# Performance work log

Measured on AMD Instinct MI355X. Metric: run time of the kernel, lower is better.

## Reference

```python
import jax, jax.numpy as jnp
import numpy as np

N = 100000      # num nodes
E = 500000      # num edges
IN_DIM = 128
OUT_DIM = 128
H = 8           # n_heads
DK = OUT_DIM // H  # 16


def setup_inputs() -> dict:
    key = jax.random.key(0)
    ks = jax.random.split(key, 16)
    s = 1.0 / np.sqrt(IN_DIM)
    inp = {
        "x": jax.random.normal(ks[0], (N, IN_DIM), dtype=jnp.float32),
        "edge_index": jax.random.randint(ks[1], (2, E), 0, N, dtype=jnp.int64),
        # per-type linear layers (num_types=1)
        "Wk": jax.random.uniform(ks[2], (OUT_DIM, IN_DIM), jnp.float32, -s, s),
        "bk": jnp.zeros((OUT_DIM,), jnp.float32),
        "Wq": jax.random.uniform(ks[3], (OUT_DIM, IN_DIM), jnp.float32, -s, s),
        "bq": jnp.zeros((OUT_DIM,), jnp.float32),
        "Wv": jax.random.uniform(ks[4], (OUT_DIM, IN_DIM), jnp.float32, -s, s),
        "bv": jnp.zeros((OUT_DIM,), jnp.float32),
        "Wa": jax.random.uniform(ks[5], (OUT_DIM, OUT_DIM), jnp.float32, -s, s),
        "ba": jnp.zeros((OUT_DIM,), jnp.float32),
        # per-relation params (num_relations=1), xavier-uniform for d_k x d_k mats
        "R_att": jax.random.uniform(ks[6], (H, DK, DK), jnp.float32, -np.sqrt(6.0 / (2 * DK)), np.sqrt(6.0 / (2 * DK))),
        "R_msg": jax.random.uniform(ks[7], (H, DK, DK), jnp.float32, -np.sqrt(6.0 / (2 * DK)), np.sqrt(6.0 / (2 * DK))),
        "R_pri": jnp.ones((H,), jnp.float32),
        "skip": jnp.ones((), jnp.float32),
    }
    return inp


def reference(x, edge_index, Wk, bk, Wq, bq, Wv, bv, Wa, ba, R_att, R_msg, R_pri, skip):
    sqrt_dk = jnp.asarray(np.sqrt(DK), x.dtype)
    # per-node projections -> [N, H, DK]
    k = (x @ Wk.T + bk).reshape(N, H, DK)
    q = (x @ Wq.T + bq).reshape(N, H, DK)
    v = (x @ Wv.T + bv).reshape(N, H, DK)
    src, dst = edge_index[0], edge_index[1]
    # edge gather: [E, H, DK]
    ke = jnp.einsum('ehd,hdf->ehf', k[src], R_att)
    ve = jnp.einsum('ehd,hdf->ehf', v[src], R_msg)
    qe = q[dst]
    # attention scores [E, H]; softmax over the edge axis (as in the original)
    att = jnp.sum(qe * ke, axis=-1) * R_pri / sqrt_dk
    att = jax.nn.softmax(att, axis=0)
    # weighted sum over all edges -> [H, DK] -> [OUT_DIM]
    out = jnp.einsum('eh,ehf->hf', att, ve).reshape(-1)
    out = Wa @ out + ba  # a_linear on the pooled vector
    alpha = jax.nn.sigmoid(skip)
    # broadcast skip mix against node inputs -> [N, OUT_DIM]
    return out * alpha + x * (1.0 - alpha)
```

## Files before the change

kernel.cpp:

```cpp
#include <hip/hip_runtime.h>
#include <hip/hip_bf16.h>

#define NN 100000
#define EE 500000
#define NB2 256
#define EGRID 2048

typedef __attribute__((ext_vector_type(8))) __bf16 bf16x8;
typedef __attribute__((ext_vector_type(4))) float f32x4;
typedef __attribute__((ext_vector_type(2))) float f32x2;

static const long long OFF_KQ8  = 0;
static const long long OFF_VB   = 6400000;
static const long long OFF_WGT  = 12800000;
static const long long OFF_PART = 13600000;
static const long long OFF_OUTV = 13634816;
static const long long OFF_CNT  = 13634944;

__device__ inline unsigned short f2bf(float f) {
    unsigned int u = __float_as_uint(f);
    unsigned int r = (u + 0x7FFFu + ((u >> 16) & 1u)) >> 16;
    return (unsigned short)r;
}
__device__ inline unsigned int pack2bf(float a, float b) {
    return (unsigned int)f2bf(a) | ((unsigned int)f2bf(b) << 16);
}
#define LOF(u) __uint_as_float((u) << 16)
#define HIF(u) __uint_as_float((u) & 0xffff0000u)

#if __has_builtin(__builtin_amdgcn_cvt_pk_fp8_f32) && __has_builtin(__builtin_amdgcn_cvt_pk_f32_fp8)
#define HW_FP8 1
#endif

__device__ inline unsigned char enc_fp8(float f) {
#ifdef HW_FP8
    int p = __builtin_amdgcn_cvt_pk_fp8_f32(f, f, 0, false);
    return (unsigned char)(p & 0xff);
#else
    unsigned int u = __float_as_uint(f);
    unsigned int s = (u >> 24) & 0x80u;
    unsigned int a = u & 0x7fffffffu;
    if (a >= 0x43e80000u) return (unsigned char)(s | 0x7e);
    if (a < 0x3c800000u) {
        float av = __uint_as_float(a);
        unsigned int m = (unsigned int)rintf(av * 512.0f);
        return (unsigned char)(s | m);
    }
    unsigned int base = a - 0x3c000000u;
    unsigned int r = (base + 0x7ffffu + ((base >> 20) & 1u)) >> 20;
    return (unsigned char)(s | r);
#endif
}

#ifndef HW_FP8
__device__ inline float dec1_fp8(unsigned int b) {
    unsigned int s = (b & 0x80u) << 24;
    unsigned int em = b & 0x7fu;
    float v;
    if (em >= 8u) v = __uint_as_float(s | ((em + 960u) << 20));
    else {
        v = (float)em * 0.001953125f;
        v = __uint_as_float(__float_as_uint(v) | s);
    }
    return v;
}
#endif

__device__ inline float dot4_fp8(unsigned int ka, unsigned int qa, float d) {
#ifdef HW_FP8
    f32x2 k0 = __builtin_amdgcn_cvt_pk_f32_fp8((int)ka, false);
    f32x2 k1 = __builtin_amdgcn_cvt_pk_f32_fp8((int)ka, true);
    f32x2 q0 = __builtin_amdgcn_cvt_pk_f32_fp8((int)qa, false);
    f32x2 q1 = __builtin_amdgcn_cvt_pk_f32_fp8((int)qa, true);
    d = fmaf(k0.x, q0.x, d); d = fmaf(k0.y, q0.y, d);
    d = fmaf(k1.x, q1.x, d); d = fmaf(k1.y, q1.y, d);
    return d;
#else
    #pragma unroll
    for (int i = 0; i < 4; ++i)
        d = fmaf(dec1_fp8((ka >> (8*i)) & 0xff), dec1_fp8((qa >> (8*i)) & 0xff), d);
    return d;
#endif
}

__global__ __launch_bounds__(512) void proj_all(const float* __restrict__ x,
                                                const float* __restrict__ Wk, const float* __restrict__ bk,
                                                const float* __restrict__ Wq, const float* __restrict__ bq,
                                                const float* __restrict__ Wv, const float* __restrict__ bv,
                                                const float* __restrict__ R_att,
                                                unsigned char* __restrict__ kq8,
                                                unsigned char* __restrict__ vb,
                                                float* __restrict__ Wgt,
                                                unsigned int* __restrict__ counter) {
    __shared__ __align__(16) char smem[131072];
    unsigned short* As = (unsigned short*)smem;
    unsigned short* Bs = (unsigned short*)(smem + 32768);
    int tid = threadIdx.x;
    long long row0 = (long long)blockIdx.x * 128;

    {
        long long zidx = (long long)blockIdx.x * 512 + tid;
        if (zidx < 200000) ((float4*)Wgt)[zidx] = make_float4(0.f, 0.f, 0.f, 0.f);
        if (blockIdx.x == 0 && tid == 0) *counter = 0u;
    }

    for (int c = tid; c < 2048; c += 512) {
        int r = c >> 4, sl = c & 15;
        long long gr = row0 + r;
        float4 v0, v1;
        if (gr < NN) {
            const float4* xp = (const float4*)(x + gr * 128 + sl * 8);
            v0 = xp[0]; v1 = xp[1];
        } else {
            v0 = make_float4(0.f, 0.f, 0.f, 0.f);
            v1 = make_float4(0.f, 0.f, 0.f, 0.f);
        }
        uint4 pk;
        pk.x = pack2bf(v0.x, v0.y); pk.y = pack2bf(v0.z, v0.w);
        pk.z = pack2bf(v1.x, v1.y); pk.w = pack2bf(v1.z, v1.w);
        *(uint4*)(As + r * 128 + (sl ^ (r & 15)) * 8) = pk;
    }
    for (int c = tid; c < 6144; c += 512) {
        int r = c >> 4, sl = c & 15;
        int cc = sl * 8;
        float w0,w1,w2,w3,w4,w5,w6,w7;
        if (r < 128) {
            float4 a = *(const float4*)(Wk + r * 128 + cc);
            float4 b = *(const float4*)(Wk + r * 128 + cc + 4);
            w0=a.x; w1=a.y; w2=a.z; w3=a.w; w4=b.x; w5=b.y; w6=b.z; w7=b.w;
        } else if (r < 256) {
            int h = (r - 128) >> 4, d = (r - 128) & 15;
            const float* Rrow = R_att + h * 256 + d * 16;
            w0=w1=w2=w3=w4=w5=w6=w7 = 0.f;
            #pragma unroll
            for (int f = 0; f < 16; ++f) {
                float rv = Rrow[f];
                const float* wq = Wq + (h * 16 + f) * 128 + cc;
                float4 a = *(const float4*)wq;
                float4 b = *(const float4*)(wq + 4);
                w0 = fmaf(rv, a.x, w0); w1 = fmaf(rv, a.y, w1);
                w2 = fmaf(rv, a.z, w2); w3 = fmaf(rv, a.w, w3);
                w4 = fmaf(rv, b.x, w4); w5 = fmaf(rv, b.y, w5);
                w6 = fmaf(rv, b.z, w6); w7 = fmaf(rv, b.w, w7);
            }
        } else {
            float4 a = *(const float4*)(Wv + (r - 256) * 128 + cc);
            float4 b = *(const float4*)(Wv + (r - 256) * 128 + cc + 4);
            w0=a.x; w1=a.y; w2=a.z; w3=a.w; w4=b.x; w5=b.y; w6=b.z; w7=b.w;
        }
        uint4 pk;
        pk.x = pack2bf(w0, w1); pk.y = pack2bf(w2, w3);
        pk.z = pack2bf(w4, w5); pk.w = pack2bf(w6, w7);
        *(uint4*)(Bs + r * 128 + (sl ^ (r & 15)) * 8) = pk;
    }
    __syncthreads();

    int lane = tid & 63, wv = tid >> 6, wr = wv >> 2, wc = wv & 3;
    int lrow = lane & 15, lk = lane >> 4;
    f32x4 acc[4][6];
    #pragma unroll
    for (int m = 0; m < 4; ++m)
        #pragma unroll
        for (int n = 0; n < 6; ++n)
            acc[m][n] = f32x4{0.f, 0.f, 0.f, 0.f};

    #pragma unroll
    for (int kk = 0; kk < 4; ++kk) {
        int kc = kk * 4 + lk;
        bf16x8 a[4], b[6];
        #pragma unroll
        for (int m = 0; m < 4; ++m) {
            int r = wr * 64 + m * 16 + lrow;
            a[m] = *(const bf16x8*)(As + r * 128 + (kc ^ (r & 15)) * 8);
        }
        #pragma unroll
        for (int n = 0; n < 6; ++n) {
            int r = wc * 96 + n * 16 + lrow;
            b[n] = *(const bf16x8*)(Bs + r * 128 + (kc ^ (r & 15)) * 8);
        }
        #pragma unroll
        for (int m = 0; m < 4; ++m)
            #pragma unroll
            for (int n = 0; n < 6; ++n)
                acc[m][n] = __builtin_amdgcn_mfma_f32_16x16x32_bf16(a[m], b[n], acc[m][n], 0, 0, 0);
    }
    __syncthreads();

    unsigned char* CsK = (unsigned char*)smem;
    unsigned short* CsV = (unsigned short*)(smem + 32768);
    float bias[6];
    #pragma unroll
    for (int n = 0; n < 6; ++n) {
        int cb = wc * 96 + n * 16 + lrow;
        if (cb < 128) bias[n] = bk[cb];
        else if (cb < 256) {
            int h = (cb - 128) >> 4, d = (cb - 128) & 15;
            float s = 0.f;
            #pragma unroll
            for (int f = 0; f < 16; ++f)
                s = fmaf(R_att[h * 256 + d * 16 + f], bq[h * 16 + f], s);
            bias[n] = s;
        } else bias[n] = bv[cb - 256];
    }
    #pragma unroll
    for (int m = 0; m < 4; ++m) {
        int rb = wr * 64 + m * 16 + lk * 4;
        #pragma unroll
        for (int n = 0; n < 6; ++n) {
            int cb = wc * 96 + n * 16 + lrow;
            if (cb < 256) {
                #pragma unroll
                for (int r = 0; r < 4; ++r)
                    CsK[(rb + r) * 256 + cb] = enc_fp8(acc[m][n][r] + bias[n]);
            } else {
                #pragma unroll
                for (int r = 0; r < 4; ++r)
                    CsV[(rb + r) * 128 + (cb - 256)] = f2bf(acc[m][n][r] + bias[n]);
            }
        }
    }
    __syncthreads();
    for (int c = tid; c < 2048; c += 512) {
        int r = c >> 4, sl = c & 15;
        long long gr = row0 + r;
        if (gr < NN)
            *(uint4*)(kq8 + gr * 256 + sl * 16) = *(const uint4*)(CsK + r * 256 + sl * 16);
    }
    for (int c = tid; c < 2048; c += 512) {
        int r = c >> 4, sl = c & 15;
        long long gr = row0 + r;
        if (gr < NN)
            *(uint4*)(vb + gr * 256 + sl * 16) = *(const uint4*)((const char*)CsV + r * 256 + sl * 16);
    }
}

__global__ __launch_bounds__(256) void edge_score(const int* __restrict__ ei,
                                                  const unsigned char* __restrict__ kq8,
                                                  const float* __restrict__ R_pri,
                                                  float* __restrict__ Wgt) {
    __shared__ unsigned int pr[256];
    int tid = threadIdx.x;
    const unsigned int* wrd = (const unsigned int*)ei;
    pr[tid] = wrd[2 * tid + 1];
    __syncthreads();
    for (int st = 128; st > 0; st >>= 1) {
        if (tid < st) pr[tid] |= pr[tid + st];
        __syncthreads();
    }
    bool is64 = (pr[0] == 0u);
    int h = tid & 7, es = tid >> 3;
    float rp = R_pri[h] * 0.25f;
    for (int base = blockIdx.x * 32; base < EE; base += EGRID * 32) {
        int e = base + es;
        if (e >= EE) continue;
        int sn, dn;
        if (is64) { sn = ei[2 * e]; dn = ei[2 * (EE + e)]; }
        else      { sn = ei[e];     dn = ei[EE + e]; }
        uint4 kw = *(const uint4*)(kq8 + (size_t)sn * 256 + h * 16);
        uint4 qw = *(const uint4*)(kq8 + (size_t)dn * 256 + 128 + h * 16);
        float d = 0.f;
        d = dot4_fp8(kw.x, qw.x, d); d = dot4_fp8(kw.y, qw.y, d);
        d = dot4_fp8(kw.z, qw.z, d); d = dot4_fp8(kw.w, qw.w, d);
        float w = __expf(d * rp);
        atomicAdd(&Wgt[(size_t)sn * 8 + h], w);
    }
}

__global__ __launch_bounds__(256) void pool_fin(const float* __restrict__ Wgt,
                                                const unsigned char* __restrict__ vb,
                                                float* __restrict__ partial,
                                                unsigned int* __restrict__ counter,
                                                const float* __restrict__ R_msg,
                                                const float* __restrict__ Wa,
                                                const float* __restrict__ ba,
                                                const float* __restrict__ skip,
                                                float* __restrict__ outv) {
    __shared__ float red[256][2];
    __shared__ float redz[256];
    int tid = threadIdx.x;
    int wv = tid >> 6, lane = tid & 63;
    int h = lane >> 3, dp = lane & 7;
    float ax = 0.f, ay = 0.f, zacc = 0.f;
    for (int n = blockIdx.x * 4 + wv; n < NN; n += NB2 * 4) {
        unsigned int vvp = *(const unsigned int*)(vb + (size_t)n * 256 + lane * 4);
        float w = Wgt[(size_t)n * 8 + h];
        ax = fmaf(w, LOF(vvp), ax);
        ay = fmaf(w, HIF(vvp), ay);
        if (dp == 0) zacc += w;
    }
    red[tid][0] = ax; red[tid][1] = ay;
    redz[tid] = (dp == 0) ? zacc : 0.f;
    __syncthreads();
    if (tid < 64) {
        float s0 = red[tid][0] + red[tid+64][0] + red[tid+128][0] + red[tid+192][0];
        float s1 = red[tid][1] + red[tid+64][1] + red[tid+128][1] + red[tid+192][1];
        partial[blockIdx.x * 136 + tid * 2]     = s0;
        partial[blockIdx.x * 136 + tid * 2 + 1] = s1;
        if ((tid & 7) == 0) {
            float z = redz[tid] + redz[tid+64] + redz[tid+128] + redz[tid+192];
            partial[blockIdx.x * 136 + 128 + (tid >> 3)] = z;
        }
    }
    __threadfence();
    __shared__ int amLast;
    if (tid == 0) amLast = (atomicAdd(counter, 1u) == NB2 - 1) ? 1 : 0;
    __syncthreads();
    if (!amLast) return;
    __threadfence();

    __shared__ float poolZ[136];
    for (int c = tid; c < 136; c += 256) {
        float s = 0.f;
        for (int b = 0; b < NB2; ++b) s += partial[b * 136 + c];
        poolZ[c] = s;
    }
    __syncthreads();
    __shared__ float pn[128];
    if (tid < 128) pn[tid] = poolZ[tid] / poolZ[128 + (tid >> 4)];
    __syncthreads();
    __shared__ float msg[128];
    if (tid < 128) {
        int hh = tid >> 4, f = tid & 15;
        float s = 0.f;
        #pragma unroll
        for (int d2 = 0; d2 < 16; ++d2)
            s = fmaf(pn[hh * 16 + d2], R_msg[hh * 256 + d2 * 16 + f], s);
        msg[tid] = s;
    }
    __syncthreads();
    if (tid < 128) {
        float s = ba[tid];
        for (int j = 0; j < 128; ++j) s = fmaf(Wa[tid * 128 + j], msg[j], s);
        float alpha = 1.f / (1.f + __expf(-skip[0]));
        outv[tid] = s * alpha;
    }
}

__global__ __launch_bounds__(256) void broadcast_out(const float* __restrict__ x,
                                                     const float* __restrict__ outv,
                                                     const float* __restrict__ skip,
                                                     float* __restrict__ out) {
    float alpha = 1.f / (1.f + __expf(-skip[0]));
    float beta = 1.f - alpha;
    const int total4 = NN * 128 / 4;
    for (int i = blockIdx.x * blockDim.x + threadIdx.x; i < total4;
         i += gridDim.x * blockDim.x) {
        float4 xv = ((const float4*)x)[i];
        int c4 = i & 31;
        float4 ov = ((const float4*)outv)[c4];
        float4 r;
        r.x = ov.x + beta * xv.x;
        r.y = ov.y + beta * xv.y;
        r.z = ov.z + beta * xv.z;
        r.w = ov.w + beta * xv.w;
        ((float4*)out)[i] = r;
    }
}

extern "C" void kernel_launch(void* const* d_in, const int* in_sizes, int n_in,
                              void* d_out, int out_size, void* d_ws, size_t ws_size,
                              hipStream_t stream) {
    const float* x      = (const float*)d_in[0];
    const int*   ei     = (const int*)d_in[1];
    const float* Wk     = (const float*)d_in[2];
    const float* bk     = (const float*)d_in[3];
    const float* Wq     = (const float*)d_in[4];
    const float* bq     = (const float*)d_in[5];
    const float* Wv     = (const float*)d_in[6];
    const float* bv     = (const float*)d_in[7];
    const float* Wa     = (const float*)d_in[8];
    const float* ba     = (const float*)d_in[9];
    const float* R_att  = (const float*)d_in[10];
    const float* R_msg  = (const float*)d_in[11];
    const float* R_pri  = (const float*)d_in[12];
    const float* skip   = (const float*)d_in[13];
    float* out = (float*)d_out;
    float* ws  = (float*)d_ws;

    unsigned char* kq8 = (unsigned char*)(ws + OFF_KQ8);
    unsigned char* vbp = (unsigned char*)(ws + OFF_VB);
    float* Wgt   = ws + OFF_WGT;
    float* part  = ws + OFF_PART;
    float* outv  = ws + OFF_OUTV;
    unsigned int* counter = (unsigned int*)(ws + OFF_CNT);

    proj_all<<<(NN + 127) / 128, 512, 0, stream>>>(x, Wk, bk, Wq, bq, Wv, bv, R_att,
                                                   kq8, vbp, Wgt, counter);
    edge_score<<<EGRID, 256, 0, stream>>>(ei, kq8, R_pri, Wgt);
    pool_fin<<<NB2, 256, 0, stream>>>(Wgt, vbp, part, counter, R_msg, Wa, ba, skip, outv);
    broadcast_out<<<2048, 256, 0, stream>>>(x, outv, skip, out);
}
```

Before: 291.5 us.

## Split projection into weight-prep kernel and column-split MFMA kernel reading x directly

The fused weight (including R_att folded into Wq) and the biases are now computed once by a small prep kernel and stored in MFMA fragment order. Previously every one of the ~782 blocks rebuilt them into LDS. The projection kernel becomes a smaller 64-row by 128-column tile over a 3-way column grid, loading A fragments straight from global x and B fragments straight from the pre-swizzled buffer, with no LDS staging for the inputs. This removes redundant per-block weight construction and the large LDS footprint, which should raise occupancy. In exchange, x is read three times (once per column group) and there is an extra kernel launch.

```diff
diff --git a/kernel.cpp b/kernel.cpp
--- a/kernel.cpp
+++ b/kernel.cpp
@@ -16,6 +16,8 @@
 static const long long OFF_PART = 13600000;
 static const long long OFF_OUTV = 13634816;
 static const long long OFF_CNT  = 13634944;
+static const long long OFF_WF   = 13635008;
+static const long long OFF_BALL = 13659584;
 
 __device__ inline unsigned short f2bf(float f) {
     unsigned int u = __float_as_uint(f);
@@ -83,154 +85,144 @@
 #endif
 }
 
-__global__ __launch_bounds__(512) void proj_all(const float* __restrict__ x,
-                                                const float* __restrict__ Wk, const float* __restrict__ bk,
-                                                const float* __restrict__ Wq, const float* __restrict__ bq,
-                                                const float* __restrict__ Wv, const float* __restrict__ bv,
-                                                const float* __restrict__ R_att,
-                                                unsigned char* __restrict__ kq8,
-                                                unsigned char* __restrict__ vb,
-                                                float* __restrict__ Wgt,
-                                                unsigned int* __restrict__ counter) {
-    __shared__ __align__(16) char smem[131072];
-    unsigned short* As = (unsigned short*)smem;
-    unsigned short* Bs = (unsigned short*)(smem + 32768);
+__global__ void prep(const float* __restrict__ Wk, const float* __restrict__ bk,
+                     const float* __restrict__ Wq, const float* __restrict__ bq,
+                     const float* __restrict__ Wv, const float* __restrict__ bv,
+                     const float* __restrict__ R_att,
+                     unsigned short* __restrict__ Wf, float* __restrict__ ball,
+                     float* __restrict__ Wgt, unsigned int* __restrict__ counter) {
+    int j = blockIdx.x;
+    int c = threadIdx.x;
+    float w;
+    if (j < 128) {
+        w = Wk[j * 128 + c];
+        if (c == 0) ball[j] = bk[j];
+    } else if (j < 256) {
+        int h = (j - 128) >> 4, d = (j - 128) & 15;
+        const float* Rrow = R_att + h * 256 + d * 16;
+        float s = 0.f;
+        #pragma unroll
+        for (int f = 0; f < 16; ++f)
+            s = fmaf(Rrow[f], Wq[(h * 16 + f) * 128 + c], s);
+        w = s;
+        if (c == 0) {
+            float sb = 0.f;
+            for (int f = 0; f < 16; ++f)
+                sb = fmaf(Rrow[f], bq[h * 16 + f], sb);
+            ball[j] = sb;
+        }
+    } else {
+        w = Wv[(j - 256) * 128 + c];
+        if (c == 0) ball[j] = bv[j - 256];
+    }
+    int g = j >> 7, wc = (j >> 6) & 1, n = (j >> 4) & 3, lr = j & 15;
+    int kk = c >> 5, lk = (c >> 3) & 3, i = c & 7;
+    int idx = ((((g * 2 + wc) * 4 + n) * 4 + kk) * 64 + lk * 16 + lr) * 8 + i;
+    Wf[idx] = f2bf(w);
+    for (int z = j * 128 + c; z < 200000; z += 384 * 128)
+        ((float4*)Wgt)[z] = make_float4(0.f, 0.f, 0.f, 0.f);
+    if (j == 0 && c == 0) *counter = 0u;
+}
+
+__global__ __launch_bounds__(256) void proj_mfma(const float* __restrict__ x,
+                                                 const unsigned short* __restrict__ Wf,
+                                                 const float* __restrict__ ball,
+                                                 unsigned char* __restrict__ kq8,
+                                                 unsigned char* __restrict__ vb) {
+    __shared__ __align__(16) char cs[16384];
     int tid = threadIdx.x;
-    long long row0 = (long long)blockIdx.x * 128;
-
-    {
-        long long zidx = (long long)blockIdx.x * 512 + tid;
-        if (zidx < 200000) ((float4*)Wgt)[zidx] = make_float4(0.f, 0.f, 0.f, 0.f);
-        if (blockIdx.x == 0 && tid == 0) *counter = 0u;
-    }
-
-    for (int c = tid; c < 2048; c += 512) {
-        int r = c >> 4, sl = c & 15;
-        long long gr = row0 + r;
-        float4 v0, v1;
-        if (gr < NN) {
-            const float4* xp = (const float4*)(x + gr * 128 + sl * 8);
-            v0 = xp[0]; v1 = xp[1];
-        } else {
-            v0 = make_float4(0.f, 0.f, 0.f, 0.f);
-            v1 = make_float4(0.f, 0.f, 0.f, 0.f);
-        }
-        uint4 pk;
-        pk.x = pack2bf(v0.x, v0.y); pk.y = pack2bf(v0.z, v0.w);
-        pk.z = pack2bf(v1.x, v1.y); pk.w = pack2bf(v1.z, v1.w);
-        *(uint4*)(As + r * 128 + (sl ^ (r & 15)) * 8) = pk;
-    }
-    for (int c = tid; c < 6144; c += 512) {
-        int r = c >> 4, sl = c & 15;
-        int cc = sl * 8;
-        float w0,w1,w2,w3,w4,w5,w6,w7;
-        if (r < 128) {
-            float4 a = *(const float4*)(Wk + r * 128 + cc);
-            float4 b = *(const float4*)(Wk + r * 128 + cc + 4);
-            w0=a.x; w1=a.y; w2=a.z; w3=a.w; w4=b.x; w5=b.y; w6=b.z; w7=b.w;
-        } else if (r < 256) {
-            int h = (r - 128) >> 4, d = (r - 128) & 15;
-            const float* Rrow = R_att + h * 256 + d * 16;
-            w0=w1=w2=w3=w4=w5=w6=w7 = 0.f;
+    int lane = tid & 63, wv = tid >> 6, wr = wv >> 1, wc = wv & 1;
+    int lrow = lane & 15, lk = lane >> 4;
+    long long row0 = (long long)blockIdx.x * 64;
+    int g = blockIdx.y;
+    int col0 = g * 128;
+
+    const float* xr[2];
+    #pragma unroll
+    for (int m = 0; m < 2; ++m) {
+        long long gr = row0 + wr * 32 + m * 16 + lrow;
+        if (gr >= NN) gr = NN - 1;
+        xr[m] = x + gr * 128;
+    }
+    const unsigned short* bfb = Wf + (size_t)((g * 2 + wc) * 16) * 512 + lane * 8;
+
+    f32x4 acc[2][4];
+    #pragma unroll
+    for (int m = 0; m < 2; ++m)
+        #pragma unroll
+        for (int n = 0; n < 4; ++n)
+            acc[m][n] = f32x4{0.f, 0.f, 0.f, 0.f};
+
+    #pragma unroll
+    for (int kk = 0; kk < 4; ++kk) {
+        bf16x8 a[2], b[4];
+        #pragma unroll
+        for (int m = 0; m < 2; ++m) {
+            const float4* p = (const float4*)(xr[m] + (kk * 4 + lk) * 8);
+            float4 u0 = p[0], u1 = p[1];
+            union { uint4 u; bf16x8 v; } cv;
+            cv.u.x = pack2bf(u0.x, u0.y); cv.u.y = pack2bf(u0.z, u0.w);
+            cv.u.z = pack2bf(u1.x, u1.y); cv.u.w = pack2bf(u1.z, u1.w);
+            a[m] = cv.v;
+        }
+        #pragma unroll
+        for (int n = 0; n < 4; ++n)
+            b[n] = *(const bf16x8*)(bfb + (size_t)(n * 4 + kk) * 512);
+        #pragma unroll
+        for (int m = 0; m < 2; ++m)
             #pragma unroll
-            for (int f = 0; f < 16; ++f) {
-                float rv = Rrow[f];
-                const float* wq = Wq + (h * 16 + f) * 128 + cc;
-                float4 a = *(const float4*)wq;
-                float4 b = *(const float4*)(wq + 4);
-                w0 = fmaf(rv, a.x, w0); w1 = fmaf(rv, a.y, w1);
-                w2 = fmaf(rv, a.z, w2); w3 = fmaf(rv, a.w, w3);
-                w4 = fmaf(rv, b.x, w4); w5 = fmaf(rv, b.y, w5);
-                w6 = fmaf(rv, b.z, w6); w7 = fmaf(rv, b.w, w7);
-            }
-        } else {
-            float4 a = *(const float4*)(Wv + (r - 256) * 128 + cc);
-            float4 b = *(const float4*)(Wv + (r - 256) * 128 + cc + 4);
-            w0=a.x; w1=a.y; w2=a.z; w3=a.w; w4=b.x; w5=b.y; w6=b.z; w7=b.w;
-        }
-        uint4 pk;
-        pk.x = pack2bf(w0, w1); pk.y = pack2bf(w2, w3);
-        pk.z = pack2bf(w4, w5); pk.w = pack2bf(w6, w7);
-        *(uint4*)(Bs + r * 128 + (sl ^ (r & 15)) * 8) = pk;
-    }
-    __syncthreads();
-
-    int lane = tid & 63, wv = tid >> 6, wr = wv >> 2, wc = wv & 3;
-    int lrow = lane & 15, lk = lane >> 4;
-    f32x4 acc[4][6];
-    #pragma unroll
-    for (int m = 0; m < 4; ++m)
-        #pragma unroll
-        for (int n = 0; n < 6; ++n)
-            acc[m][n] = f32x4{0.f, 0.f, 0.f, 0.f};
-
-    #pragma unroll
-    for (int kk = 0; kk < 4; ++kk) {
-        int kc = kk * 4 + lk;
-        bf16x8 a[4], b[6];
-        #pragma unroll
-        for (int m = 0; m < 4; ++m) {
-            int r = wr * 64 + m * 16 + lrow;
-            a[m] = *(const bf16x8*)(As + r * 128 + (kc ^ (r & 15)) * 8);
-        }
-        #pragma unroll
-        for (int n = 0; n < 6; ++n) {
-            int r = wc * 96 + n * 16 + lrow;
-            b[n] = *(const bf16x8*)(Bs + r * 128 + (kc ^ (r & 15)) * 8);
-        }
-        #pragma unroll
-        for (int m = 0; m < 4; ++m)
+            for (int n = 0; n < 4; ++n)
+                acc[m][n] = __builtin_amdgcn_mfma_f32_16x16x32_bf16(a[m], b[n], acc[m][n], 0, 0, 0);
+    }
+
+    float bias[4];
+    #pragma unroll
+    for (int n = 0; n < 4; ++n) bias[n] = ball[col0 + wc * 64 + n * 16 + lrow];
+
+    if (g < 2) {
+        unsigned char* C = (unsigned char*)cs;
+        #pragma unroll
+        for (int m = 0; m < 2; ++m) {
+            int rb = wr * 32 + m * 16 + lk * 4;
             #pragma unroll
-            for (int n = 0; n < 6; ++n)
-                acc[m][n] = __builtin_amdgcn_mfma_f32_16x16x32_bf16(a[m], b[n], acc[m][n], 0, 0, 0);
-    }
-    __syncthreads();
-
-    unsigned char* CsK = (unsigned char*)smem;
-    unsigned short* CsV = (unsigned short*)(smem + 32768);
-    float bias[6];
-    #pragma unroll
-    for (int n = 0; n < 6; ++n) {
-        int cb = wc * 96 + n * 16 + lrow;
-        if (cb < 128) bias[n] = bk[cb];
-        else if (cb < 256) {
-            int h = (cb - 128) >> 4, d = (cb - 128) & 15;
-            float s = 0.f;
-            #pragma unroll
-            for (int f = 0; f < 16; ++f)
-                s = fmaf(R_att[h * 256 + d * 16 + f], bq[h * 16 + f], s);
-            bias[n] = s;
-        } else bias[n] = bv[cb - 256];
-    }
-    #pragma unroll
-    for (int m = 0; m < 4; ++m) {
-        int rb = wr * 64 + m * 16 + lk * 4;
-        #pragma unroll
-        for (int n = 0; n < 6; ++n) {
-            int cb = wc * 96 + n * 16 + lrow;
-            if (cb < 256) {
+            for (int n = 0; n < 4; ++n) {
+                int cb = wc * 64 + n * 16 + lrow;
                 #pragma unroll
                 for (int r = 0; r < 4; ++r)
-                    CsK[(rb + r) * 256 + cb] = enc_fp8(acc[m][n][r] + bias[n]);
-            } else {
+                    C[(rb + r) * 128 + cb] = enc_fp8(acc[m][n][r] + bias[n]);
+            }
+        }
+        __syncthreads();
+        #pragma unroll
+        for (int it = 0; it < 2; ++it) {
+            int c = tid + it * 256;
+            int r = c >> 3, sl = c & 7;
+            long long gr = row0 + r;
+            if (gr < NN)
+                *(uint4*)(kq8 + gr * 256 + col0 + sl * 16) = *(const uint4*)(C + r * 128 + sl * 16);
+        }
+    } else {
+        unsigned short* C = (unsigned short*)cs;
+        #pragma unroll
+        for (int m = 0; m < 2; ++m) {
+            int rb = wr * 32 + m * 16 + lk * 4;
+            #pragma unroll
+            for (int n = 0; n < 4; ++n) {
+                int cb = wc * 64 + n * 16 + lrow;
                 #pragma unroll
                 for (int r = 0; r < 4; ++r)
-                    CsV[(rb + r) * 128 + (cb - 256)] = f2bf(acc[m][n][r] + bias[n]);
+                    C[(rb + r) * 128 + cb] = f2bf(acc[m][n][r] + bias[n]);
             }
         }
-    }
-    __syncthreads();
-    for (int c = tid; c < 2048; c += 512) {
-        int r = c >> 4, sl = c & 15;
-        long long gr = row0 + r;
-        if (gr < NN)
-            *(uint4*)(kq8 + gr * 256 + sl * 16) = *(const uint4*)(CsK + r * 256 + sl * 16);
-    }
-    for (int c = tid; c < 2048; c += 512) {
-        int r = c >> 4, sl = c & 15;
-        long long gr = row0 + r;
-        if (gr < NN)
-            *(uint4*)(vb + gr * 256 + sl * 16) = *(const uint4*)((const char*)CsV + r * 256 + sl * 16);
+        __syncthreads();
+        #pragma unroll
+        for (int it = 0; it < 4; ++it) {
+            int c = tid + it * 256;
+            int r = c >> 4, sl = c & 15;
+            long long gr = row0 + r;
+            if (gr < NN)
+                *(uint4*)(vb + gr * 256 + sl * 16) = *(const uint4*)((const char*)C + r * 256 + sl * 16);
+        }
     }
 }
 
@@ -383,9 +375,12 @@
     float* part  = ws + OFF_PART;
     float* outv  = ws + OFF_OUTV;
     unsigned int* counter = (unsigned int*)(ws + OFF_CNT);
-
-    proj_all<<<(NN + 127) / 128, 512, 0, stream>>>(x, Wk, bk, Wq, bq, Wv, bv, R_att,
-                                                   kq8, vbp, Wgt, counter);
+    unsigned short* Wf = (unsigned short*)(ws + OFF_WF);
+    float* ball  = ws + OFF_BALL;
+
+    prep<<<384, 128, 0, stream>>>(Wk, bk, Wq, bq, Wv, bv, R_att, Wf, ball, Wgt, counter);
+    dim3 gg((NN + 63) / 64, 3);
+    proj_mfma<<<gg, 256, 0, stream>>>(x, Wf, ball, kq8, vbp);
     edge_score<<<EGRID, 256, 0, stream>>>(ei, kq8, R_pri, Wgt);
     pool_fin<<<NB2, 256, 0, stream>>>(Wgt, vbp, part, counter, R_msg, Wa, ba, skip, outv);
     broadcast_out<<<2048, 256, 0, stream>>>(x, outv, skip, out);
```

Result: faster. 261.9 us (-10.2%).
